# Kernel optimization log

Measured on AMD Instinct MI355X. Metric: run time of the kernel, lower is better.

## Reference

```python
import jax, jax.numpy as jnp
import numpy as np

EPS = 1e-6
N_SINKHORN = 5
NEG_SLOPE = 0.01


def setup_inputs() -> dict:
    key = jax.random.key(0)
    ks = jax.random.split(key, 12)
    N, D, H, A, L = 262144, 256, 256, 64, 128

    def lin(kw, kb, fan_in, shape_w, shape_b):
        b = 1.0 / np.sqrt(fan_in)
        w = jax.random.uniform(kw, shape_w, jnp.float32, -b, b)
        bb = jax.random.uniform(kb, shape_b, jnp.float32, -b, b)
        return w, bb

    k0_w, k0_b = lin(ks[0], ks[1], D, (H, D), (H,))
    k1_w, k1_b = lin(ks[2], ks[3], H, (A, H), (A,))
    q0_w, q0_b = lin(ks[4], ks[5], D, (H, D), (H,))
    q1_w, q1_b = lin(ks[6], ks[7], H, (A, H), (A,))
    return {
        "yhat_embedding": jax.random.normal(ks[8], (N, D), jnp.float32),
        "y_embedding": jax.random.normal(ks[9], (N, D), jnp.float32),
        "k0_w": k0_w, "k0_b": k0_b, "k1_w": k1_w, "k1_b": k1_b,
        "q0_w": q0_w, "q0_b": q0_b, "q1_w": q1_w, "q1_b": q1_b,
        "seg_len": L,
    }


def reference(yhat_embedding, y_embedding, k0_w, k0_b, k1_w, k1_b,
              q0_w, q0_b, q1_w, q1_b, seg_len):
    N, D = y_embedding.shape
    n_seg = N // seg_len
    y = y_embedding.reshape(n_seg, seg_len, D)    # [s, l, D]
    yh = yhat_embedding.reshape(n_seg, seg_len, D)

    leaky = lambda x: jax.nn.leaky_relu(x, NEG_SLOPE)
    # k path: k1(leaky(k0(y)))
    k = leaky(jnp.einsum('sld,hd->slh', y, k0_w) + k0_b)
    k = jnp.einsum('slh,ah->sla', k, k1_w) + k1_b        # [s, l, A]
    # q path: q1(leaky(q0(yhat)))
    q = leaky(jnp.einsum('sld,hd->slh', yh, q0_w) + q0_b)
    q = jnp.einsum('slh,ah->sla', q, q1_w) + q1_b        # [s, l, A]

    M = jnp.einsum('sla,sma->slm', k, q)                 # [s, l, l]
    attn = jax.nn.softmax(M, axis=2)                     # torch softmax(dim=1) per 2D mat
    loss_vec = attn.sum(axis=1) + EPS                    # sum over rows (torch axis=0)
    loss = jnp.sum(-jnp.log(loss_vec) * loss_vec)

    W = (attn + EPS) / seg_len
    dim = 1
    for _ in range(N_SINKHORN):
        dim = 1 - dim
        ax = 1 if dim == 0 else 2  # torch axis -> per-segment axis (+1)
        W = W / W.sum(axis=ax, keepdims=True)
        W = W / seg_len
    return W, loss
```

## Files before the change

kernel.cpp:

```cpp
#include <hip/hip_runtime.h>
#include <hip/hip_bf16.h>

#define NROWS 262144
#define DDIM 256
#define HDIM 256
#define ADIM 64
#define LSEG 128
#define NSEG 2048
#define EPSF 1e-6f
#define TM 64
#define NBPP 256
#define TPB 16

typedef __attribute__((ext_vector_type(8))) short bf16x8;
typedef __attribute__((ext_vector_type(4))) float f32x4;

__device__ __forceinline__ unsigned short f2bf(float x){
  unsigned u = __float_as_uint(x);
  u += 0x7FFFu + ((u >> 16) & 1u);
  return (unsigned short)(u >> 16);
}

__device__ __forceinline__ unsigned int pk2bf(float a, float b){
  union { __hip_bfloat162 h2; unsigned int u; } cv;
  cv.h2 = __float22bfloat162_rn(make_float2(a, b));
  return cv.u;
}

__device__ __forceinline__ int fragidx(int h, int k){
  return (((h >> 4)*8 + (k >> 5))*64 + ((k >> 3) & 3)*16 + (h & 15))*8 + (k & 7);
}

__device__ __forceinline__ int fragidx0(int h, int k){
  int hh = (h & ~31) | ((h & 1) << 4) | ((h & 31) >> 1);
  return fragidx(hh, k);
}

__global__ void cvt4_kernel(const float* __restrict__ s0, const float* __restrict__ s1,
                            const float* __restrict__ s2, const float* __restrict__ s3,
                            unsigned short* __restrict__ d0, unsigned short* __restrict__ d1,
                            unsigned short* __restrict__ d2, unsigned short* __restrict__ d3){
  int i = blockIdx.x * blockDim.x + threadIdx.x;
  if(i < 65536){
    d0[fragidx0(i >> 8, i & 255)] = f2bf(s0[i]);
  } else if(i < 81920){
    int j = i - 65536;
    d1[fragidx(j >> 8, j & 255)] = f2bf(s1[j]);
  } else if(i < 147456){
    int j = i - 81920;
    d2[fragidx0(j >> 8, j & 255)] = f2bf(s2[j]);
  } else {
    int j = i - 147456;
    d3[fragidx(j >> 8, j & 255)] = f2bf(s3[j]);
  }
}

__global__ __launch_bounds__(512, 2) void mlp_kernel(
    const float* __restrict__ Xk, const float* __restrict__ Xq,
    const unsigned short* __restrict__ W0k, const float* __restrict__ B0k,
    const unsigned short* __restrict__ W1k, const float* __restrict__ B1k,
    const unsigned short* __restrict__ W0q, const float* __restrict__ B0q,
    const unsigned short* __restrict__ W1q, const float* __restrict__ B1q,
    unsigned short* __restrict__ OUTk, unsigned short* __restrict__ OUTq)
{
  __shared__ __align__(16) unsigned short xls[2][TM * 264];
  __shared__ __align__(16) float b1s[ADIM];

  const int tid  = threadIdx.x;
  const int lane = tid & 63;
  const int wid  = tid >> 6;
  const bool qpath = blockIdx.x >= NBPP;
  const int  bp   = blockIdx.x & (NBPP - 1);

  const float* X = qpath ? Xq : Xk;
  const unsigned short* W0p = qpath ? W0q : W0k;
  const float* B0 = qpath ? B0q : B0k;
  const unsigned short* W1p = qpath ? W1q : W1k;
  const float* B1 = qpath ? B1q : B1k;
  unsigned short* OUT = qpath ? OUTq : OUTk;

  const int frow = lane & 15;
  const int kg   = lane >> 4;
  const int koff = kg * 8;
  const int crow = kg * 4;
  const int ccol = frow;

  if(tid < ADIM) b1s[tid] = B1[tid];

  bf16x8 w0f[8][2];
  #pragma unroll
  for(int ks=0; ks<8; ++ks)
    #pragma unroll
    for(int htl=0; htl<2; ++htl)
      w0f[ks][htl] = *reinterpret_cast<const bf16x8*>(
          W0p + (((wid*2 + htl)*8 + ks)*64 + lane)*8);

  const float2 b0p = *reinterpret_cast<const float2*>(&B0[wid*32 + 2*ccol]);
  const int rt  = wid >> 1;
  const int at0 = (wid & 1) * 2;

  float4 xr[8];
  {
    const float4* Xv = reinterpret_cast<const float4*>(X + (size_t)bp * TM * DDIM);
    #pragma unroll
    for(int it=0; it<8; ++it) xr[it] = Xv[it*512 + tid];
    #pragma unroll
    for(int it=0; it<8; ++it){
      int idx = it*512 + tid;
      int r = idx >> 6, c4 = idx & 63;
      uint2 pk = { pk2bf(xr[it].x, xr[it].y), pk2bf(xr[it].z, xr[it].w) };
      *reinterpret_cast<uint2*>(&xls[0][r*264 + c4*4]) = pk;
    }
  }
  __syncthreads();

  for(int t=0; t<TPB; ++t){
    const int cur = t & 1;
    const size_t row0 = ((size_t)bp + (size_t)t * NBPP) * TM;

    if(t < TPB-1){
      const float4* Xn = reinterpret_cast<const float4*>(
          X + ((size_t)bp + (size_t)(t+1) * NBPP) * TM * DDIM);
      #pragma unroll
      for(int it=0; it<8; ++it) xr[it] = Xn[it*512 + tid];
    }

    f32x4 acc[4][2];
    #pragma unroll
    for(int m=0;m<4;++m){ acc[m][0] = (f32x4){0.f,0.f,0.f,0.f};
                          acc[m][1] = (f32x4){0.f,0.f,0.f,0.f}; }
    const unsigned short* xc = xls[cur];
    #pragma unroll
    for(int ks=0; ks<8; ++ks){
      bf16x8 a[4];
      #pragma unroll
      for(int mt=0; mt<4; ++mt)
        a[mt] = *reinterpret_cast<const bf16x8*>(&xc[(mt*16 + frow)*264 + ks*32 + koff]);
      #pragma unroll
      for(int mt=0; mt<4; ++mt){
        acc[mt][0] = __builtin_amdgcn_mfma_f32_16x16x32_bf16(a[mt], w0f[ks][0], acc[mt][0], 0, 0, 0);
        acc[mt][1] = __builtin_amdgcn_mfma_f32_16x16x32_bf16(a[mt], w0f[ks][1], acc[mt][1], 0, 0, 0);
      }
    }
    __syncthreads();

    unsigned short* hc = xls[cur];
    #pragma unroll
    for(int mt=0; mt<4; ++mt){
      #pragma unroll
      for(int r=0; r<4; ++r){
        float x0 = acc[mt][0][r] + b0p.x;
        float x1 = acc[mt][1][r] + b0p.y;
        x0 = x0 > 0.f ? x0 : 0.01f * x0;
        x1 = x1 > 0.f ? x1 : 0.01f * x1;
        *reinterpret_cast<unsigned int*>(
            &hc[(mt*16 + crow + r)*264 + wid*32 + 2*ccol]) = pk2bf(x0, x1);
      }
    }

    if(t < TPB-1){
      #pragma unroll
      for(int it=0; it<8; ++it){
        int idx = it*512 + tid;
        int r = idx >> 6, c4 = idx & 63;
        uint2 pk = { pk2bf(xr[it].x, xr[it].y), pk2bf(xr[it].z, xr[it].w) };
        *reinterpret_cast<uint2*>(&xls[cur^1][r*264 + c4*4]) = pk;
      }
    }

    bf16x8 w1f[2][8];
    #pragma unroll
    for(int tt=0; tt<2; ++tt)
      #pragma unroll
      for(int ks=0; ks<8; ++ks)
        w1f[tt][ks] = *reinterpret_cast<const bf16x8*>(
            W1p + (((at0+tt)*8 + ks)*64 + lane)*8);
    __syncthreads();

    f32x4 acc2[2];
    acc2[0] = (f32x4){0.f,0.f,0.f,0.f};
    acc2[1] = (f32x4){0.f,0.f,0.f,0.f};
    #pragma unroll
    for(int ks=0; ks<8; ++ks){
      bf16x8 ah = *reinterpret_cast<const bf16x8*>(&hc[(rt*16 + frow)*264 + ks*32 + koff]);
      acc2[0] = __builtin_amdgcn_mfma_f32_16x16x32_bf16(w1f[0][ks], ah, acc2[0], 0, 0, 0);
      acc2[1] = __builtin_amdgcn_mfma_f32_16x16x32_bf16(w1f[1][ks], ah, acc2[1], 0, 0, 0);
    }
    {
      const float4 b1q0 = *reinterpret_cast<const float4*>(&b1s[(at0  )*16 + crow]);
      const float4 b1q1 = *reinterpret_cast<const float4*>(&b1s[(at0+1)*16 + crow]);
      const size_t obase = (row0 + rt*16 + ccol) * ADIM;
      uint2 o0 = { pk2bf(acc2[0][0] + b1q0.x, acc2[0][1] + b1q0.y),
                   pk2bf(acc2[0][2] + b1q0.z, acc2[0][3] + b1q0.w) };
      *reinterpret_cast<uint2*>(&OUT[obase + at0*16 + crow]) = o0;
      uint2 o1 = { pk2bf(acc2[1][0] + b1q1.x, acc2[1][1] + b1q1.y),
                   pk2bf(acc2[1][2] + b1q1.z, acc2[1][3] + b1q1.w) };
      *reinterpret_cast<uint2*>(&OUT[obase + (at0+1)*16 + crow]) = o1;
    }
  }
}

__global__ __launch_bounds__(256) void seg_kernel(
    const unsigned short* __restrict__ Kb,
    const unsigned short* __restrict__ Qb,
    float* __restrict__ Wout,
    float* __restrict__ lossp)
{
  __shared__ __align__(16) float sm[LSEG * 132];
  __shared__ float cs[LSEG];
  __shared__ float cs2[LSEG];
  const int tid  = threadIdx.x;
  const int lane = tid & 63;
  const int wid  = tid >> 6;
  const long sbase = (long)blockIdx.x * (LSEG * ADIM);

  unsigned short* kt = reinterpret_cast<unsigned short*>(sm);
  unsigned short* qt = kt + LSEG * 72;

  {
    const uint4* Kv = reinterpret_cast<const uint4*>(Kb + sbase);
    const uint4* Qv = reinterpret_cast<const uint4*>(Qb + sbase);
    #pragma unroll
    for(int it=0; it<4; ++it){
      int idx = it*256 + tid;
      int r = idx >> 3, c8 = (idx & 7) * 8;
      *reinterpret_cast<uint4*>(&kt[r*72 + c8]) = Kv[idx];
      *reinterpret_cast<uint4*>(&qt[r*72 + c8]) = Qv[idx];
    }
  }
  __syncthreads();

  const int arow = lane & 15;
  const int koff = (lane >> 4) * 8;
  f32x4 acc[8][2];
  #pragma unroll
  for(int i=0;i<8;++i){ acc[i][0] = (f32x4){0.f,0.f,0.f,0.f}; acc[i][1] = (f32x4){0.f,0.f,0.f,0.f}; }
  #pragma unroll
  for(int ks=0; ks<2; ++ks){
    bf16x8 a[8], b[2];
    #pragma unroll
    for(int mt=0;mt<8;++mt)
      a[mt] = *reinterpret_cast<const bf16x8*>(&kt[(mt*16 + arow)*72 + ks*32 + koff]);
    #pragma unroll
    for(int nt=0;nt<2;++nt)
      b[nt] = *reinterpret_cast<const bf16x8*>(&qt[(wid*32 + nt*16 + arow)*72 + ks*32 + koff]);
    #pragma unroll
    for(int mt=0;mt<8;++mt)
      #pragma unroll
      for(int nt=0;nt<2;++nt)
        acc[mt][nt] = __builtin_amdgcn_mfma_f32_16x16x32_bf16(a[mt], b[nt], acc[mt][nt], 0, 0, 0);
  }
  __syncthreads();

  const int crow = (lane >> 4) * 4;
  const int ccol = lane & 15;
  #pragma unroll
  for(int mt=0;mt<8;++mt)
    #pragma unroll
    for(int nt=0;nt<2;++nt){
      int col = wid*32 + nt*16 + ccol;
      #pragma unroll
      for(int r=0;r<4;++r)
        sm[(mt*16 + crow + r)*132 + col] = acc[mt][nt][r];
    }
  __syncthreads();

  const int row  = tid >> 1;
  const int half = tid & 1;
  float* Mrow = &sm[row*132 + half*64];
  float p[64];
  #pragma unroll
  for(int j=0;j<64;j+=4){
    float4 v = *reinterpret_cast<const float4*>(Mrow + j);
    p[j] = v.x; p[j+1] = v.y; p[j+2] = v.z; p[j+3] = v.w;
  }
  float mx = p[0];
  #pragma unroll
  for(int j=1;j<64;++j) mx = fmaxf(mx, p[j]);
  mx = fmaxf(mx, __shfl_xor(mx, 1));
  float s = 0.f;
  #pragma unroll
  for(int j=0;j<64;++j){ p[j] = __expf(p[j] - mx); s += p[j]; }
  s += __shfl_xor(s, 1);
  float inv = 1.f / s;
  #pragma unroll
  for(int j=0;j<64;++j) p[j] *= inv;
  #pragma unroll
  for(int j=0;j<64;j+=4)
    *reinterpret_cast<float4*>(Mrow + j) = make_float4(p[j], p[j+1], p[j+2], p[j+3]);
  __syncthreads();

  {
    const int col = tid & 127, hf = tid >> 7;
    float ps = 0.f;
    #pragma unroll 8
    for(int l=hf*64; l<hf*64+64; ++l) ps += sm[l*132 + col];
    if(hf) cs2[col] = ps;
    __syncthreads();
    if(tid < LSEG){
      float cssum = ps + cs2[tid];
      float v  = cssum + EPSF;
      float lp = -__logf(v) * v;
      #pragma unroll
      for(int o=1;o<64;o<<=1) lp += __shfl_xor(lp, o);
      if(lane == 0) atomicAdd(lossp, lp);
      cs[tid] = 1.f / ((cssum + 128.f * EPSF) * 128.f);
    }
  }
  __syncthreads();

  float rs = 0.f;
  #pragma unroll
  for(int j=0;j<64;++j){ p[j] = (p[j] + EPSF) * cs[half*64 + j]; rs += p[j]; }
  rs += __shfl_xor(rs, 1);
  float inv2 = 1.f / (rs * 128.f);
  #pragma unroll
  for(int j=0;j<64;++j) p[j] *= inv2;
  #pragma unroll
  for(int j=0;j<64;j+=4)
    *reinterpret_cast<float4*>(Mrow + j) = make_float4(p[j], p[j+1], p[j+2], p[j+3]);
  __syncthreads();

  {
    const int col = tid & 127, hf = tid >> 7;
    float ps = 0.f;
    #pragma unroll 8
    for(int l=hf*64; l<hf*64+64; ++l) ps += sm[l*132 + col];
    if(hf) cs2[col] = ps;
    __syncthreads();
    if(tid < LSEG) cs[tid] = 1.f / ((ps + cs2[tid]) * 128.f);
  }
  __syncthreads();

  rs = 0.f;
  #pragma unroll
  for(int j=0;j<64;++j){ p[j] *= cs[half*64 + j]; rs += p[j]; }
  rs += __shfl_xor(rs, 1);
  float inv4 = 1.f / (rs * 128.f);
  #pragma unroll
  for(int j=0;j<64;++j) p[j] *= inv4;
  #pragma unroll
  for(int j=0;j<64;j+=4)
    *reinterpret_cast<float4*>(Mrow + j) = make_float4(p[j], p[j+1], p[j+2], p[j+3]);
  __syncthreads();

  {
    const int col = tid & 127, hf = tid >> 7;
    float ps = 0.f;
    #pragma unroll 8
    for(int l=hf*64; l<hf*64+64; ++l) ps += sm[l*132 + col];
    if(hf) cs2[col] = ps;
    __syncthreads();
    if(tid < LSEG) cs[tid] = 1.f / ((ps + cs2[tid]) * 128.f);
  }
  __syncthreads();

  float* outseg = Wout + (long)blockIdx.x * (LSEG*LSEG);
  #pragma unroll
  for(int it=0; it<16; ++it){
    int f = it*1024 + tid*4;
    int r = f >> 7, c = f & 127;
    float4 v = *reinterpret_cast<const float4*>(&sm[r*132 + c]);
    v.x *= cs[c]; v.y *= cs[c+1]; v.z *= cs[c+2]; v.w *= cs[c+3];
    *reinterpret_cast<float4*>(outseg + f) = v;
  }
}

extern "C" void kernel_launch(void* const* d_in, const int* in_sizes, int n_in,
                              void* d_out, int out_size, void* d_ws, size_t ws_size,
                              hipStream_t stream) {
  (void)in_sizes; (void)n_in; (void)ws_size;
  const float* yhat = (const float*)d_in[0];
  const float* y    = (const float*)d_in[1];
  const float* k0w  = (const float*)d_in[2];
  const float* k0b  = (const float*)d_in[3];
  const float* k1w  = (const float*)d_in[4];
  const float* k1b  = (const float*)d_in[5];
  const float* q0w  = (const float*)d_in[6];
  const float* q0b  = (const float*)d_in[7];
  const float* q1w  = (const float*)d_in[8];
  const float* q1b  = (const float*)d_in[9];

  unsigned short* Kbuf = (unsigned short*)d_ws;
  unsigned short* Qbuf = Kbuf + (size_t)NROWS * ADIM;
  unsigned short* w0k  = Qbuf + (size_t)NROWS * ADIM;
  unsigned short* w1k  = w0k + HDIM * DDIM;
  unsigned short* w0q  = w1k + ADIM * HDIM;
  unsigned short* w1q  = w0q + HDIM * DDIM;

  cvt4_kernel<<<640, 256, 0, stream>>>(k0w, k1w, q0w, q1w, w0k, w1k, w0q, w1q);

  mlp_kernel<<<2 * NBPP, 512, 0, stream>>>(y, yhat,
                                           w0k, k0b, w1k, k1b,
                                           w0q, q0b, w1q, q1b,
                                           Kbuf, Qbuf);

  float* Wout  = (float*)d_out;
  float* lossp = Wout + (size_t)(out_size - 1);
  hipMemsetAsync(lossp, 0, sizeof(float), stream);
  seg_kernel<<<NSEG, 256, 0, stream>>>(Kbuf, Qbuf, Wout, lossp);
}
```

Before: 216.0 us.

## Fuse MLP projection and per-segment softmax/Sinkhorn into one kernel

```diff
diff --git a/kernel.cpp b/kernel.cpp
--- a/kernel.cpp
+++ b/kernel.cpp
@@ -9,8 +9,6 @@
 #define NSEG 2048
 #define EPSF 1e-6f
 #define TM 64
-#define NBPP 256
-#define TPB 16
 
 typedef __attribute__((ext_vector_type(8))) short bf16x8;
 typedef __attribute__((ext_vector_type(4))) float f32x4;
@@ -55,37 +53,38 @@
   }
 }
 
-__global__ __launch_bounds__(512, 2) void mlp_kernel(
+__global__ __launch_bounds__(512, 2) void fused_kernel(
     const float* __restrict__ Xk, const float* __restrict__ Xq,
     const unsigned short* __restrict__ W0k, const float* __restrict__ B0k,
     const unsigned short* __restrict__ W1k, const float* __restrict__ B1k,
     const unsigned short* __restrict__ W0q, const float* __restrict__ B0q,
     const unsigned short* __restrict__ W1q, const float* __restrict__ B1q,
-    unsigned short* __restrict__ OUTk, unsigned short* __restrict__ OUTq)
+    float* __restrict__ Wout, float* __restrict__ lossp)
 {
-  __shared__ __align__(16) unsigned short xls[2][TM * 264];
-  __shared__ __align__(16) float b1s[ADIM];
+  __shared__ __align__(16) unsigned char ldsraw[TM*264*2 + 2*LSEG*72*2];
+  __shared__ float cs[LSEG];
+  __shared__ float cs2[LSEG];
+  __shared__ __align__(16) float b1s[2][ADIM];
+
+  unsigned short* xbuf = reinterpret_cast<unsigned short*>(ldsraw);
+  unsigned short* kqb  = reinterpret_cast<unsigned short*>(ldsraw + TM*264*2);
+  float* sm = reinterpret_cast<float*>(ldsraw);
 
   const int tid  = threadIdx.x;
   const int lane = tid & 63;
   const int wid  = tid >> 6;
-  const bool qpath = blockIdx.x >= NBPP;
-  const int  bp   = blockIdx.x & (NBPP - 1);
-
-  const float* X = qpath ? Xq : Xk;
-  const unsigned short* W0p = qpath ? W0q : W0k;
-  const float* B0 = qpath ? B0q : B0k;
-  const unsigned short* W1p = qpath ? W1q : W1k;
-  const float* B1 = qpath ? B1q : B1k;
-  unsigned short* OUT = qpath ? OUTq : OUTk;
 
   const int frow = lane & 15;
   const int kg   = lane >> 4;
   const int koff = kg * 8;
   const int crow = kg * 4;
   const int ccol = frow;
-
-  if(tid < ADIM) b1s[tid] = B1[tid];
+  const int rt  = wid >> 1;
+  const int at0 = (wid & 1) * 2;
+
+  if(tid < 2*ADIM) b1s[tid >> 6][tid & 63] = (tid < ADIM ? B1k : B1q)[tid & 63];
+
+  const size_t rbase = (size_t)blockIdx.x * LSEG;
 
   bf16x8 w0f[8][2];
   #pragma unroll
@@ -93,49 +92,57 @@
     #pragma unroll
     for(int htl=0; htl<2; ++htl)
       w0f[ks][htl] = *reinterpret_cast<const bf16x8*>(
-          W0p + (((wid*2 + htl)*8 + ks)*64 + lane)*8);
-
-  const float2 b0p = *reinterpret_cast<const float2*>(&B0[wid*32 + 2*ccol]);
-  const int rt  = wid >> 1;
-  const int at0 = (wid & 1) * 2;
+          W0k + (((wid*2 + htl)*8 + ks)*64 + lane)*8);
+  float2 b0p = *reinterpret_cast<const float2*>(&B0k[wid*32 + 2*ccol]);
 
   float4 xr[8];
   {
-    const float4* Xv = reinterpret_cast<const float4*>(X + (size_t)bp * TM * DDIM);
+    const float4* Xv = reinterpret_cast<const float4*>(Xk + rbase * DDIM);
     #pragma unroll
     for(int it=0; it<8; ++it) xr[it] = Xv[it*512 + tid];
+  }
+
+  for(int t=0; t<4; ++t){
+    const int th = t & 1;
+    (void)th;
+
+    if(t == 2){
+      #pragma unroll
+      for(int ks=0; ks<8; ++ks)
+        #pragma unroll
+        for(int htl=0; htl<2; ++htl)
+          w0f[ks][htl] = *reinterpret_cast<const bf16x8*>(
+              W0q + (((wid*2 + htl)*8 + ks)*64 + lane)*8);
+      b0p = *reinterpret_cast<const float2*>(&B0q[wid*32 + 2*ccol]);
+    }
+
     #pragma unroll
     for(int it=0; it<8; ++it){
       int idx = it*512 + tid;
       int r = idx >> 6, c4 = idx & 63;
       uint2 pk = { pk2bf(xr[it].x, xr[it].y), pk2bf(xr[it].z, xr[it].w) };
-      *reinterpret_cast<uint2*>(&xls[0][r*264 + c4*4]) = pk;
-    }
-  }
-  __syncthreads();
-
-  for(int t=0; t<TPB; ++t){
-    const int cur = t & 1;
-    const size_t row0 = ((size_t)bp + (size_t)t * NBPP) * TM;
-
-    if(t < TPB-1){
-      const float4* Xn = reinterpret_cast<const float4*>(
-          X + ((size_t)bp + (size_t)(t+1) * NBPP) * TM * DDIM);
-      #pragma unroll
-      for(int it=0; it<8; ++it) xr[it] = Xn[it*512 + tid];
-    }
+      *reinterpret_cast<uint2*>(&xbuf[r*264 + c4*4]) = pk;
+    }
+
+    if(t < 3){
+      const float* Xn = (((t+1) >> 1) ? Xq : Xk);
+      const float4* Xv = reinterpret_cast<const float4*>(
+          Xn + (rbase + (size_t)((t+1) & 1) * TM) * DDIM);
+      #pragma unroll
+      for(int it=0; it<8; ++it) xr[it] = Xv[it*512 + tid];
+    }
+    __syncthreads();
 
     f32x4 acc[4][2];
     #pragma unroll
     for(int m=0;m<4;++m){ acc[m][0] = (f32x4){0.f,0.f,0.f,0.f};
                           acc[m][1] = (f32x4){0.f,0.f,0.f,0.f}; }
-    const unsigned short* xc = xls[cur];
     #pragma unroll
     for(int ks=0; ks<8; ++ks){
       bf16x8 a[4];
       #pragma unroll
       for(int mt=0; mt<4; ++mt)
-        a[mt] = *reinterpret_cast<const bf16x8*>(&xc[(mt*16 + frow)*264 + ks*32 + koff]);
+        a[mt] = *reinterpret_cast<const bf16x8*>(&xbuf[(mt*16 + frow)*264 + ks*32 + koff]);
       #pragma unroll
       for(int mt=0; mt<4; ++mt){
         acc[mt][0] = __builtin_amdgcn_mfma_f32_16x16x32_bf16(a[mt], w0f[ks][0], acc[mt][0], 0, 0, 0);
@@ -144,7 +151,6 @@
     }
     __syncthreads();
 
-    unsigned short* hc = xls[cur];
     #pragma unroll
     for(int mt=0; mt<4; ++mt){
       #pragma unroll
@@ -154,20 +160,11 @@
         x0 = x0 > 0.f ? x0 : 0.01f * x0;
         x1 = x1 > 0.f ? x1 : 0.01f * x1;
         *reinterpret_cast<unsigned int*>(
-            &hc[(mt*16 + crow + r)*264 + wid*32 + 2*ccol]) = pk2bf(x0, x1);
+            &xbuf[(mt*16 + crow + r)*264 + wid*32 + 2*ccol]) = pk2bf(x0, x1);
       }
     }
 
-    if(t < TPB-1){
-      #pragma unroll
-      for(int it=0; it<8; ++it){
-        int idx = it*512 + tid;
-        int r = idx >> 6, c4 = idx & 63;
-        uint2 pk = { pk2bf(xr[it].x, xr[it].y), pk2bf(xr[it].z, xr[it].w) };
-        *reinterpret_cast<uint2*>(&xls[cur^1][r*264 + c4*4]) = pk;
-      }
-    }
-
+    const unsigned short* W1p = ((t >> 1) ? W1q : W1k);
     bf16x8 w1f[2][8];
     #pragma unroll
     for(int tt=0; tt<2; ++tt)
@@ -182,120 +179,102 @@
     acc2[1] = (f32x4){0.f,0.f,0.f,0.f};
     #pragma unroll
     for(int ks=0; ks<8; ++ks){
-      bf16x8 ah = *reinterpret_cast<const bf16x8*>(&hc[(rt*16 + frow)*264 + ks*32 + koff]);
+      bf16x8 ah = *reinterpret_cast<const bf16x8*>(&xbuf[(rt*16 + frow)*264 + ks*32 + koff]);
       acc2[0] = __builtin_amdgcn_mfma_f32_16x16x32_bf16(w1f[0][ks], ah, acc2[0], 0, 0, 0);
       acc2[1] = __builtin_amdgcn_mfma_f32_16x16x32_bf16(w1f[1][ks], ah, acc2[1], 0, 0, 0);
     }
     {
-      const float4 b1q0 = *reinterpret_cast<const float4*>(&b1s[(at0  )*16 + crow]);
-      const float4 b1q1 = *reinterpret_cast<const float4*>(&b1s[(at0+1)*16 + crow]);
-      const size_t obase = (row0 + rt*16 + ccol) * ADIM;
+      const float4 b1q0 = *reinterpret_cast<const float4*>(&b1s[t >> 1][(at0  )*16 + crow]);
+      const float4 b1q1 = *reinterpret_cast<const float4*>(&b1s[t >> 1][(at0+1)*16 + crow]);
+      unsigned short* kqp = kqb + (t >> 1) * (LSEG * 72);
+      const int orow = (t & 1)*TM + rt*16 + ccol;
       uint2 o0 = { pk2bf(acc2[0][0] + b1q0.x, acc2[0][1] + b1q0.y),
                    pk2bf(acc2[0][2] + b1q0.z, acc2[0][3] + b1q0.w) };
-      *reinterpret_cast<uint2*>(&OUT[obase + at0*16 + crow]) = o0;
+      *reinterpret_cast<uint2*>(&kqp[orow*72 + at0*16 + crow]) = o0;
       uint2 o1 = { pk2bf(acc2[1][0] + b1q1.x, acc2[1][1] + b1q1.y),
                    pk2bf(acc2[1][2] + b1q1.z, acc2[1][3] + b1q1.w) };
-      *reinterpret_cast<uint2*>(&OUT[obase + (at0+1)*16 + crow]) = o1;
-    }
-  }
-}
-
-__global__ __launch_bounds__(256) void seg_kernel(
-    const unsigned short* __restrict__ Kb,
-    const unsigned short* __restrict__ Qb,
-    float* __restrict__ Wout,
-    float* __restrict__ lossp)
-{
-  __shared__ __align__(16) float sm[LSEG * 132];
-  __shared__ float cs[LSEG];
-  __shared__ float cs2[LSEG];
-  const int tid  = threadIdx.x;
-  const int lane = tid & 63;
-  const int wid  = tid >> 6;
-  const long sbase = (long)blockIdx.x * (LSEG * ADIM);
-
-  unsigned short* kt = reinterpret_cast<unsigned short*>(sm);
-  unsigned short* qt = kt + LSEG * 72;
-
-  {
-    const uint4* Kv = reinterpret_cast<const uint4*>(Kb + sbase);
-    const uint4* Qv = reinterpret_cast<const uint4*>(Qb + sbase);
-    #pragma unroll
-    for(int it=0; it<4; ++it){
-      int idx = it*256 + tid;
-      int r = idx >> 3, c8 = (idx & 7) * 8;
-      *reinterpret_cast<uint4*>(&kt[r*72 + c8]) = Kv[idx];
-      *reinterpret_cast<uint4*>(&qt[r*72 + c8]) = Qv[idx];
-    }
-  }
-  __syncthreads();
-
-  const int arow = lane & 15;
-  const int koff = (lane >> 4) * 8;
-  f32x4 acc[8][2];
-  #pragma unroll
-  for(int i=0;i<8;++i){ acc[i][0] = (f32x4){0.f,0.f,0.f,0.f}; acc[i][1] = (f32x4){0.f,0.f,0.f,0.f}; }
-  #pragma unroll
-  for(int ks=0; ks<2; ++ks){
-    bf16x8 a[8], b[2];
-    #pragma unroll
-    for(int mt=0;mt<8;++mt)
-      a[mt] = *reinterpret_cast<const bf16x8*>(&kt[(mt*16 + arow)*72 + ks*32 + koff]);
-    #pragma unroll
-    for(int nt=0;nt<2;++nt)
-      b[nt] = *reinterpret_cast<const bf16x8*>(&qt[(wid*32 + nt*16 + arow)*72 + ks*32 + koff]);
-    #pragma unroll
-    for(int mt=0;mt<8;++mt)
-      #pragma unroll
-      for(int nt=0;nt<2;++nt)
-        acc[mt][nt] = __builtin_amdgcn_mfma_f32_16x16x32_bf16(a[mt], b[nt], acc[mt][nt], 0, 0, 0);
-  }
-  __syncthreads();
-
-  const int crow = (lane >> 4) * 4;
-  const int ccol = lane & 15;
-  #pragma unroll
-  for(int mt=0;mt<8;++mt)
-    #pragma unroll
-    for(int nt=0;nt<2;++nt){
-      int col = wid*32 + nt*16 + ccol;
-      #pragma unroll
-      for(int r=0;r<4;++r)
-        sm[(mt*16 + crow + r)*132 + col] = acc[mt][nt][r];
-    }
-  __syncthreads();
-
-  const int row  = tid >> 1;
-  const int half = tid & 1;
-  float* Mrow = &sm[row*132 + half*64];
+      *reinterpret_cast<uint2*>(&kqp[orow*72 + (at0+1)*16 + crow]) = o1;
+    }
+    __syncthreads();
+  }
+
+  unsigned short* kt = kqb;
+  unsigned short* qt = kqb + LSEG * 72;
+
+  {
+    f32x4 sacc[8][2];
+    if(tid < 256){
+      const int arow = lane & 15;
+      #pragma unroll
+      for(int i=0;i<8;++i){ sacc[i][0] = (f32x4){0.f,0.f,0.f,0.f}; sacc[i][1] = (f32x4){0.f,0.f,0.f,0.f}; }
+      #pragma unroll
+      for(int ks=0; ks<2; ++ks){
+        bf16x8 a[8], b[2];
+        #pragma unroll
+        for(int mt=0;mt<8;++mt)
+          a[mt] = *reinterpret_cast<const bf16x8*>(&kt[(mt*16 + arow)*72 + ks*32 + koff]);
+        #pragma unroll
+        for(int nt=0;nt<2;++nt)
+          b[nt] = *reinterpret_cast<const bf16x8*>(&qt[(wid*32 + nt*16 + arow)*72 + ks*32 + koff]);
+        #pragma unroll
+        for(int mt=0;mt<8;++mt)
+          #pragma unroll
+          for(int nt=0;nt<2;++nt)
+            sacc[mt][nt] = __builtin_amdgcn_mfma_f32_16x16x32_bf16(a[mt], b[nt], sacc[mt][nt], 0, 0, 0);
+      }
+    }
+    __syncthreads();
+
+    if(tid < 256){
+      const int scrow = (lane >> 4) * 4;
+      const int sccol = lane & 15;
+      #pragma unroll
+      for(int mt=0;mt<8;++mt)
+        #pragma unroll
+        for(int nt=0;nt<2;++nt){
+          int col = wid*32 + nt*16 + sccol;
+          #pragma unroll
+          for(int r=0;r<4;++r)
+            sm[(mt*16 + scrow + r)*132 + col] = sacc[mt][nt][r];
+        }
+    }
+  }
+  __syncthreads();
+
   float p[64];
-  #pragma unroll
-  for(int j=0;j<64;j+=4){
-    float4 v = *reinterpret_cast<const float4*>(Mrow + j);
-    p[j] = v.x; p[j+1] = v.y; p[j+2] = v.z; p[j+3] = v.w;
-  }
-  float mx = p[0];
-  #pragma unroll
-  for(int j=1;j<64;++j) mx = fmaxf(mx, p[j]);
-  mx = fmaxf(mx, __shfl_xor(mx, 1));
-  float s = 0.f;
-  #pragma unroll
-  for(int j=0;j<64;++j){ p[j] = __expf(p[j] - mx); s += p[j]; }
-  s += __shfl_xor(s, 1);
-  float inv = 1.f / s;
-  #pragma unroll
-  for(int j=0;j<64;++j) p[j] *= inv;
-  #pragma unroll
-  for(int j=0;j<64;j+=4)
-    *reinterpret_cast<float4*>(Mrow + j) = make_float4(p[j], p[j+1], p[j+2], p[j+3]);
+  if(tid < 256){
+    const int srow = tid >> 1, shalf = tid & 1;
+    float* Mrow = &sm[srow*132 + shalf*64];
+    #pragma unroll
+    for(int j=0;j<64;j+=4){
+      float4 v = *reinterpret_cast<const float4*>(Mrow + j);
+      p[j] = v.x; p[j+1] = v.y; p[j+2] = v.z; p[j+3] = v.w;
+    }
+    float mx = p[0];
+    #pragma unroll
+    for(int j=1;j<64;++j) mx = fmaxf(mx, p[j]);
+    mx = fmaxf(mx, __shfl_xor(mx, 1));
+    float s = 0.f;
+    #pragma unroll
+    for(int j=0;j<64;++j){ p[j] = __expf(p[j] - mx); s += p[j]; }
+    s += __shfl_xor(s, 1);
+    float inv = 1.f / s;
+    #pragma unroll
+    for(int j=0;j<64;++j) p[j] *= inv;
+    #pragma unroll
+    for(int j=0;j<64;j+=4)
+      *reinterpret_cast<float4*>(Mrow + j) = make_float4(p[j], p[j+1], p[j+2], p[j+3]);
+  }
   __syncthreads();
 
   {
     const int col = tid & 127, hf = tid >> 7;
     float ps = 0.f;
-    #pragma unroll 8
-    for(int l=hf*64; l<hf*64+64; ++l) ps += sm[l*132 + col];
-    if(hf) cs2[col] = ps;
+    if(tid < 256){
+      #pragma unroll 8
+      for(int l=hf*64; l<hf*64+64; ++l) ps += sm[l*132 + col];
+      if(hf) cs2[col] = ps;
+    }
     __syncthreads();
     if(tid < LSEG){
       float cssum = ps + cs2[tid];
@@ -309,47 +288,59 @@
   }
   __syncthreads();
 
-  float rs = 0.f;
-  #pragma unroll
-  for(int j=0;j<64;++j){ p[j] = (p[j] + EPSF) * cs[half*64 + j]; rs += p[j]; }
-  rs += __shfl_xor(rs, 1);
-  float inv2 = 1.f / (rs * 128.f);
-  #pragma unroll
-  for(int j=0;j<64;++j) p[j] *= inv2;
-  #pragma unroll
-  for(int j=0;j<64;j+=4)
-    *reinterpret_cast<float4*>(Mrow + j) = make_float4(p[j], p[j+1], p[j+2], p[j+3]);
+  if(tid < 256){
+    const int srow = tid >> 1, shalf = tid & 1;
+    float* Mrow = &sm[srow*132 + shalf*64];
+    float rs = 0.f;
+    #pragma unroll
+    for(int j=0;j<64;++j){ p[j] = (p[j] + EPSF) * cs[shalf*64 + j]; rs += p[j]; }
+    rs += __shfl_xor(rs, 1);
+    float inv2 = 1.f / (rs * 128.f);
+    #pragma unroll
+    for(int j=0;j<64;++j) p[j] *= inv2;
+    #pragma unroll
+    for(int j=0;j<64;j+=4)
+      *reinterpret_cast<float4*>(Mrow + j) = make_float4(p[j], p[j+1], p[j+2], p[j+3]);
+  }
   __syncthreads();
 
   {
     const int col = tid & 127, hf = tid >> 7;
     float ps = 0.f;
-    #pragma unroll 8
-    for(int l=hf*64; l<hf*64+64; ++l) ps += sm[l*132 + col];
-    if(hf) cs2[col] = ps;
+    if(tid < 256){
+      #pragma unroll 8
+      for(int l=hf*64; l<hf*64+64; ++l) ps += sm[l*132 + col];
+      if(hf) cs2[col] = ps;
+    }
     __syncthreads();
     if(tid < LSEG) cs[tid] = 1.f / ((ps + cs2[tid]) * 128.f);
   }
   __syncthreads();
 
-  rs = 0.f;
-  #pragma unroll
-  for(int j=0;j<64;++j){ p[j] *= cs[half*64 + j]; rs += p[j]; }
-  rs += __shfl_xor(rs, 1);
-  float inv4 = 1.f / (rs * 128.f);
-  #pragma unroll
-  for(int j=0;j<64;++j) p[j] *= inv4;
-  #pragma unroll
-  for(int j=0;j<64;j+=4)
-    *reinterpret_cast<float4*>(Mrow + j) = make_float4(p[j], p[j+1], p[j+2], p[j+3]);
+  if(tid < 256){
+    const int srow = tid >> 1, shalf = tid & 1;
+    float* Mrow = &sm[srow*132 + shalf*64];
+    float rs = 0.f;
+    #pragma unroll
+    for(int j=0;j<64;++j){ p[j] *= cs[shalf*64 + j]; rs += p[j]; }
+    rs += __shfl_xor(rs, 1);
+    float inv4 = 1.f / (rs * 128.f);
+    #pragma unroll
+    for(int j=0;j<64;++j) p[j] *= inv4;
+    #pragma unroll
+    for(int j=0;j<64;j+=4)
+      *reinterpret_cast<float4*>(Mrow + j) = make_float4(p[j], p[j+1], p[j+2], p[j+3]);
+  }
   __syncthreads();
 
   {
     const int col = tid & 127, hf = tid >> 7;
     float ps = 0.f;
-    #pragma unroll 8
-    for(int l=hf*64; l<hf*64+64; ++l) ps += sm[l*132 + col];
-    if(hf) cs2[col] = ps;
+    if(tid < 256){
+      #pragma unroll 8
+      for(int l=hf*64; l<hf*64+64; ++l) ps += sm[l*132 + col];
+      if(hf) cs2[col] = ps;
+    }
     __syncthreads();
     if(tid < LSEG) cs[tid] = 1.f / ((ps + cs2[tid]) * 128.f);
   }
@@ -357,8 +348,8 @@
 
   float* outseg = Wout + (long)blockIdx.x * (LSEG*LSEG);
   #pragma unroll
-  for(int it=0; it<16; ++it){
-    int f = it*1024 + tid*4;
+  for(int it=0; it<8; ++it){
+    int f = it*2048 + tid*4;
     int r = f >> 7, c = f & 127;
     float4 v = *reinterpret_cast<const float4*>(&sm[r*132 + c]);
     v.x *= cs[c]; v.y *= cs[c+1]; v.z *= cs[c+2]; v.w *= cs[c+3];
@@ -381,22 +372,19 @@
   const float* q1w  = (const float*)d_in[8];
   const float* q1b  = (const float*)d_in[9];
 
-  unsigned short* Kbuf = (unsigned short*)d_ws;
-  unsigned short* Qbuf = Kbuf + (size_t)NROWS * ADIM;
-  unsigned short* w0k  = Qbuf + (size_t)NROWS * ADIM;
-  unsigned short* w1k  = w0k + HDIM * DDIM;
-  unsigned short* w0q  = w1k + ADIM * HDIM;
-  unsigned short* w1q  = w0q + HDIM * DDIM;
-
-  cvt4_kernel<<<640, 256, 0, stream>>>(k0w, k1w, q0w, q1w, w0k, w1k, w0q, w1q);
-
-  mlp_kernel<<<2 * NBPP, 512, 0, stream>>>(y, yhat,
-                                           w0k, k0b, w1k, k1b,
-                                           w0q, q0b, w1q, q1b,
-                                           Kbuf, Qbuf);
+  unsigned short* w0k = (unsigned short*)d_ws;
+  unsigned short* w1k = w0k + HDIM * DDIM;
+  unsigned short* w0q = w1k + ADIM * HDIM;
+  unsigned short* w1q = w0q + HDIM * DDIM;
 
   float* Wout  = (float*)d_out;
   float* lossp = Wout + (size_t)(out_size - 1);
   hipMemsetAsync(lossp, 0, sizeof(float), stream);
-  seg_kernel<<<NSEG, 256, 0, stream>>>(Kbuf, Qbuf, Wout, lossp);
-}
+
+  cvt4_kernel<<<640, 256, 0, stream>>>(k0w, k1w, q0w, q1w, w0k, w1k, w0q, w1q);
+
+  fused_kernel<<<NSEG, 512, 0, stream>>>(y, yhat,
+                                         w0k, k0b, w1k, k1b,
+                                         w0q, q0b, w1q, q1b,
+                                         Wout, lossp);
+}
```

Measured after the change: 250.4 us. 1.16x slower.
